# Kernel optimization log

Measured on AMD Instinct MI355X. Metric: run time of the kernel, lower is better.

## Reference

```python
import jax, jax.numpy as jnp
import numpy as np

EMBED_DIM = 1024
NUM_HEADS = 16
HEAD_DIM = EMBED_DIM // NUM_HEADS
LN_EPS = 1e-12
B, S = 2, 2048


def setup_inputs() -> dict:
    key = jax.random.key(0)
    ks = jax.random.split(key, 12)
    scale = 1.0 / np.sqrt(EMBED_DIM)
    d = EMBED_DIM
    return {
        "in_features": jax.random.normal(ks[0], (B, S, d), dtype=jnp.float32),
        "tgt_mask": jnp.ones((B, S), dtype=jnp.float32),
        "Wq": jax.random.normal(ks[1], (d, d), dtype=jnp.float32) * scale,
        "bq": jnp.zeros((d,), dtype=jnp.float32),
        "Wk": jax.random.normal(ks[2], (d, d), dtype=jnp.float32) * scale,
        "bk": jnp.zeros((d,), dtype=jnp.float32),
        "Wv": jax.random.normal(ks[3], (d, d), dtype=jnp.float32) * scale,
        "bv": jnp.zeros((d,), dtype=jnp.float32),
        "Wo": jax.random.normal(ks[4], (d, d), dtype=jnp.float32) * scale,
        "bo": jnp.zeros((d,), dtype=jnp.float32),
        "gamma": jnp.ones((d,), dtype=jnp.float32),
        "beta": jnp.zeros((d,), dtype=jnp.float32),
    }


def _split_heads(x):  # [B,S,D] -> [B,H,S,Dh]
    b, s, _ = x.shape
    return x.reshape(b, s, NUM_HEADS, HEAD_DIM).transpose(0, 2, 1, 3)


def reference(in_features, tgt_mask, Wq, bq, Wk, bk, Wv, bv, Wo, bo, gamma, beta):
    # Self-attention (tgt_features defaults to in_features). Dropout in eval mode (identity).
    q = _split_heads(in_features @ Wq.T + bq)
    k = _split_heads(in_features @ Wk.T + bk)
    v = _split_heads(in_features @ Wv.T + bv)
    # scores: [B,H,S,S]
    scores = jnp.einsum("bhqd,bhkd->bhqk", q, k) / jnp.sqrt(jnp.float32(HEAD_DIM))
    scores = scores + (1.0 - tgt_mask)[:, None, None, :] * (-100000.0)
    attn = jax.nn.softmax(scores, axis=-1)
    ctx = jnp.einsum("bhqk,bhkd->bhqd", attn, v)  # [B,H,S,Dh]
    ctx = ctx.transpose(0, 2, 1, 3).reshape(in_features.shape)  # merge heads
    out = ctx @ Wo.T + bo
    x = out + in_features
    mu = jnp.mean(x, axis=-1, keepdims=True)
    var = jnp.mean(jnp.square(x - mu), axis=-1, keepdims=True)
    return (x - mu) / jnp.sqrt(var + LN_EPS) * gamma + beta
```

## Files before the change

### kernel.cpp

```cpp
#include <hip/hip_runtime.h>
#include <hip/hip_bf16.h>

#define DM   1024
#define HEADS 16
#define DH    64
#define SEQ  2048
#define BATCH   2
#define LOG2E 1.44269504088896f

typedef __attribute__((ext_vector_type(8))) short short8;
typedef __attribute__((ext_vector_type(4))) short bf16x4;
typedef __attribute__((ext_vector_type(4))) float floatx4;

__device__ __forceinline__ short f2b(float f) {
    union { float f; unsigned u; } v; v.f = f;
    unsigned r = v.u + 0x7FFFu + ((v.u >> 16) & 1u);
    return (short)(r >> 16);
}

#if __has_builtin(__builtin_amdgcn_exp2f)
__device__ __forceinline__ float fexp2(float x) { return __builtin_amdgcn_exp2f(x); }
#else
__device__ __forceinline__ float fexp2(float x) { return exp2f(x); }
#endif

__device__ __forceinline__ void async_copy16(const short* gsrc, short* ldst) {
    __builtin_amdgcn_global_load_lds(
        (const __attribute__((address_space(1))) void*)gsrc,
        (__attribute__((address_space(3))) void*)ldst,
        16, 0, 0);
}

__global__ __launch_bounds__(256) void cvt_all(const float* __restrict__ x,
        const float* __restrict__ wq, const float* __restrict__ wk,
        const float* __restrict__ wv, const float* __restrict__ wo,
        const float* __restrict__ mask,
        short* __restrict__ xb, short* __restrict__ wqkv, short* __restrict__ wob,
        float* __restrict__ maddg)
{
    const int b = blockIdx.x;
    if (b >= 8192) {
        const int bb = b - 8192;
        const float* mrow = mask + (size_t)bb * SEQ;
        float* mg = maddg + (size_t)bb * SEQ;
#pragma unroll
        for (int i = 0; i < 8; ++i) {
            const int idx = threadIdx.x * 8 + i;
            mg[idx] = (1.f - mrow[idx]) * (-100000.f * LOG2E);
        }
        return;
    }
    const float* src; short* dst; int idx;
    if (b < 4096)      { src = x;  dst = xb;                idx = b; }
    else if (b < 5120) { src = wq; dst = wqkv;              idx = b - 4096; }
    else if (b < 6144) { src = wk; dst = wqkv + (1 << 20);  idx = b - 5120; }
    else if (b < 7168) { src = wv; dst = wqkv + (2 << 20);  idx = b - 6144; }
    else               { src = wo; dst = wob;               idx = b - 7168; }
    const int i = idx * 256 + threadIdx.x;
    floatx4 v = ((const floatx4*)src)[i];
    bf16x4 o;
    o.x = f2b(v.x); o.y = f2b(v.y); o.z = f2b(v.z); o.w = f2b(v.w);
    ((bf16x4*)dst)[i] = o;
}

__global__ __launch_bounds__(256) void gemm_qkv(const short* __restrict__ A,
        const short* __restrict__ B,
        const float* __restrict__ bq, const float* __restrict__ bk,
        const float* __restrict__ bv,
        short* __restrict__ qw, short* __restrict__ kw, short* __restrict__ vtw)
{
    __shared__ short As[128 * 32];
    __shared__ short Bs[128 * 32];
    const int m0 = blockIdx.x * 128, n0 = blockIdx.y * 128;
    const int w = threadIdx.x >> 6, lane = threadIdx.x & 63;
    const int l16 = lane & 15, quad = lane >> 4;
    const int wm = w >> 1, wn = w & 1;
    const int lr = lane >> 2, lc = (lane & 3) * 8;

    floatx4 acc[4][4];
#pragma unroll
    for (int i = 0; i < 4; ++i)
#pragma unroll
        for (int j = 0; j < 4; ++j) acc[i][j] = (floatx4){0.f, 0.f, 0.f, 0.f};

    for (int kt = 0; kt < DM / 32; ++kt) {
        const int k0 = kt * 32;
        __syncthreads();
        async_copy16(A + (size_t)(m0 + w * 32 + lr) * DM + k0 + lc,      &As[w * 1024]);
        async_copy16(A + (size_t)(m0 + w * 32 + 16 + lr) * DM + k0 + lc, &As[w * 1024 + 512]);
        async_copy16(B + (size_t)(n0 + w * 32 + lr) * DM + k0 + lc,      &Bs[w * 1024]);
        async_copy16(B + (size_t)(n0 + w * 32 + 16 + lr) * DM + k0 + lc, &Bs[w * 1024 + 512]);
        __syncthreads();

        short8 af[4], bf[4];
#pragma unroll
        for (int i = 0; i < 4; ++i)
            af[i] = *(const short8*)&As[(wm * 64 + i * 16 + l16) * 32 + quad * 8];
#pragma unroll
        for (int j = 0; j < 4; ++j)
            bf[j] = *(const short8*)&Bs[(wn * 64 + j * 16 + l16) * 32 + quad * 8];
#pragma unroll
        for (int i = 0; i < 4; ++i)
#pragma unroll
            for (int j = 0; j < 4; ++j)
                acc[i][j] = __builtin_amdgcn_mfma_f32_16x16x32_bf16(af[i], bf[j], acc[i][j], 0, 0, 0);
    }

    const int m_base = m0 + wm * 64 + quad * 4;
#pragma unroll
    for (int j = 0; j < 4; ++j) {
        const int nb = n0 + wn * 64 + j * 16;
        const int t = nb >> 10;
        const int nn = (nb & 1023) + l16;
        const int h = nn >> 6, dh = nn & 63;
        const float* bias = (t == 0) ? bq : (t == 1) ? bk : bv;
        const float bvv = bias[nn];
        if (t == 2) {
#pragma unroll
            for (int i = 0; i < 4; ++i) {
                const int m = m_base + i * 16;
                const int b = m >> 11, s = m & (SEQ - 1);
                bf16x4 p;
                p.x = f2b(acc[i][j][0] + bvv);
                p.y = f2b(acc[i][j][1] + bvv);
                p.z = f2b(acc[i][j][2] + bvv);
                p.w = f2b(acc[i][j][3] + bvv);
                *(bf16x4*)&vtw[(((size_t)(b * HEADS + h)) * DH + dh) * SEQ + s] = p;
            }
        } else {
            short* dst = (t == 0) ? qw : kw;
            const float mulf = (t == 0) ? (0.125f * LOG2E) : 1.0f;
#pragma unroll
            for (int i = 0; i < 4; ++i)
#pragma unroll
                for (int r = 0; r < 4; ++r) {
                    const int m = m_base + i * 16 + r;
                    const int b = m >> 11, s = m & (SEQ - 1);
                    dst[(((size_t)(b * HEADS + h)) * SEQ + s) * DH + dh] =
                        f2b((acc[i][j][r] + bvv) * mulf);
                }
        }
    }
}

__global__ __launch_bounds__(256) void attn_kernel(const short* __restrict__ q,
        const short* __restrict__ k, const short* __restrict__ vt,
        const float* __restrict__ maddg, short* __restrict__ ctx)
{
    const int qtile = blockIdx.x;
    const int bh    = blockIdx.y;
    const int bidx  = bh >> 4;
    const int wave = threadIdx.x >> 6, lane = threadIdx.x & 63;
    const int l16 = lane & 15, quad = lane >> 4;
    const int lx = l16 & 7;

    __shared__ short k_lds[2][64 * 64];
    __shared__ short v_lds[2][64 * 64];
    __shared__ short p_lds[4][16 * 64];

    const int qrow = qtile * 64 + wave * 16 + l16;
    const short* qbase = q + ((size_t)bh * SEQ + qrow) * DH;
    short8 b_q[2];
#pragma unroll
    for (int ks = 0; ks < 2; ++ks)
        b_q[ks] = *(const short8*)(qbase + ks * 32 + quad * 8);

    float m_own = -1e30f;
    floatx4 o[4];
    floatx4 l_acc = (floatx4){0.f, 0.f, 0.f, 0.f};
#pragma unroll
    for (int d = 0; d < 4; ++d) o[d] = (floatx4){0.f, 0.f, 0.f, 0.f};

    short8 ones;
#pragma unroll
    for (int j = 0; j < 8; ++j) ones[j] = (short)0x3F80;

    const short* kbase0 = k  + (size_t)bh * SEQ * DH;
    const short* vbase0 = vt + (size_t)bh * DH * SEQ;
    const float* mrow   = maddg + (size_t)bidx * SEQ;

    const int srow0 = (wave * 64 + lane) >> 3;
    const int srow1 = (256 + wave * 64 + lane) >> 3;
    const int sc    = lane & 7;
    const int g0 = sc ^ (srow0 & 7), g1 = sc ^ (srow1 & 7);

    {
        async_copy16(kbase0 + srow0 * DH + g0 * 8,        &k_lds[0][(wave * 64) * 8]);
        async_copy16(vbase0 + (size_t)srow0 * SEQ + g0 * 8, &v_lds[0][(wave * 64) * 8]);
        async_copy16(kbase0 + srow1 * DH + g1 * 8,        &k_lds[0][(256 + wave * 64) * 8]);
        async_copy16(vbase0 + (size_t)srow1 * SEQ + g1 * 8, &v_lds[0][(256 + wave * 64) * 8]);
    }

    for (int kt = 0; kt < SEQ / 64; ++kt) {
        const int cur = kt & 1;
        __syncthreads();

        floatx4 md[4];
#pragma unroll
        for (int nt = 0; nt < 4; ++nt)
            md[nt] = *(const floatx4*)&mrow[kt * 64 + nt * 16 + quad * 4];

        if (kt + 1 < SEQ / 64) {
            const short* kbase = kbase0 + (size_t)((kt + 1) * 64) * DH;
            const short* vbase = vbase0 + (kt + 1) * 64;
            const int nb = 1 - cur;
            async_copy16(kbase + srow0 * DH + g0 * 8,        &k_lds[nb][(wave * 64) * 8]);
            async_copy16(vbase + (size_t)srow0 * SEQ + g0 * 8, &v_lds[nb][(wave * 64) * 8]);
            async_copy16(kbase + srow1 * DH + g1 * 8,        &k_lds[nb][(256 + wave * 64) * 8]);
            async_copy16(vbase + (size_t)srow1 * SEQ + g1 * 8, &v_lds[nb][(256 + wave * 64) * 8]);
        }

        float sv[4][4];
#pragma unroll
        for (int nt = 0; nt < 4; ++nt) {
            floatx4 acc = md[nt];
#pragma unroll
            for (int ks = 0; ks < 2; ++ks) {
                short8 a = *(const short8*)
                    &k_lds[cur][(nt * 16 + l16) * 64 + (((ks * 4 + quad) ^ lx) * 8)];
                acc = __builtin_amdgcn_mfma_f32_16x16x32_bf16(a, b_q[ks], acc, 0, 0, 0);
            }
#pragma unroll
            for (int r = 0; r < 4; ++r) sv[nt][r] = acc[r];
        }

        float tm = sv[0][0];
#pragma unroll
        for (int nt = 0; nt < 4; ++nt)
#pragma unroll
            for (int r = 0; r < 4; ++r) tm = fmaxf(tm, sv[nt][r]);
        tm = fmaxf(tm, __shfl_xor(tm, 16));
        tm = fmaxf(tm, __shfl_xor(tm, 32));
        const int upd = __any(tm > m_own);
        const float nm = fmaxf(m_own, tm);

#pragma unroll
        for (int nt = 0; nt < 4; ++nt) {
            const float p0 = fexp2(sv[nt][0] - nm);
            const float p1 = fexp2(sv[nt][1] - nm);
            const float p2 = fexp2(sv[nt][2] - nm);
            const float p3 = fexp2(sv[nt][3] - nm);
            union { __hip_bfloat162 h[2]; bf16x4 v; } u;
            u.h[0] = __float22bfloat162_rn(make_float2(p0, p1));
            u.h[1] = __float22bfloat162_rn(make_float2(p2, p3));
            *(bf16x4*)&p_lds[wave][l16 * 64 +
                (((nt * 2 + (quad >> 1)) ^ lx) * 8) + (quad & 1) * 4] = u.v;
        }

        if (upd) {
            const float alpha = fexp2(m_own - nm);
            float ab[4];
#pragma unroll
            for (int r = 0; r < 4; ++r)
                ab[r] = __shfl(alpha, (lane & 48) | (quad * 4 + r));
#pragma unroll
            for (int d = 0; d < 4; ++d)
#pragma unroll
                for (int r = 0; r < 4; ++r) o[d][r] *= ab[r];
#pragma unroll
            for (int r = 0; r < 4; ++r) l_acc[r] *= ab[r];
        }
        m_own = nm;

#pragma unroll
        for (int ks2 = 0; ks2 < 2; ++ks2) {
            short8 pf = *(const short8*)
                &p_lds[wave][l16 * 64 + (((ks2 * 4 + quad) ^ lx) * 8)];
#pragma unroll
            for (int d = 0; d < 4; ++d) {
                short8 vf = *(const short8*)
                    &v_lds[cur][(d * 16 + l16) * 64 + (((ks2 * 4 + quad) ^ lx) * 8)];
                o[d] = __builtin_amdgcn_mfma_f32_16x16x32_bf16(pf, vf, o[d], 0, 0, 0);
            }
            l_acc = __builtin_amdgcn_mfma_f32_16x16x32_bf16(pf, ones, l_acc, 0, 0, 0);
        }
    }

    const int h = bh & 15, bb = bh >> 4;
    const int srow = qtile * 64 + wave * 16 + quad * 4;
    float rl[4];
#pragma unroll
    for (int r = 0; r < 4; ++r) rl[r] = 1.f / l_acc[r];
#pragma unroll
    for (int d = 0; d < 4; ++d) {
        const int dh = d * 16 + l16;
#pragma unroll
        for (int r = 0; r < 4; ++r) {
            const float val = o[d][r] * rl[r];
            ctx[((size_t)(bb * SEQ + srow + r)) * DM + h * 64 + dh] = f2b(val);
        }
    }
}

__global__ __launch_bounds__(256) void gemm_o(const short* __restrict__ A,
        const short* __restrict__ B, const float* __restrict__ bo,
        const float* __restrict__ xin, float* __restrict__ out)
{
    __shared__ short As[128 * 32];
    __shared__ short Bs[128 * 32];
    const int m0 = blockIdx.x * 128, n0 = blockIdx.y * 128;
    const int w = threadIdx.x >> 6, lane = threadIdx.x & 63;
    const int l16 = lane & 15, quad = lane >> 4;
    const int wm = w >> 1, wn = w & 1;
    const int lr = lane >> 2, lc = (lane & 3) * 8;

    floatx4 acc[4][4];
#pragma unroll
    for (int i = 0; i < 4; ++i)
#pragma unroll
        for (int j = 0; j < 4; ++j) acc[i][j] = (floatx4){0.f, 0.f, 0.f, 0.f};

    for (int kt = 0; kt < DM / 32; ++kt) {
        const int k0 = kt * 32;
        __syncthreads();
        async_copy16(A + (size_t)(m0 + w * 32 + lr) * DM + k0 + lc,      &As[w * 1024]);
        async_copy16(A + (size_t)(m0 + w * 32 + 16 + lr) * DM + k0 + lc, &As[w * 1024 + 512]);
        async_copy16(B + (size_t)(n0 + w * 32 + lr) * DM + k0 + lc,      &Bs[w * 1024]);
        async_copy16(B + (size_t)(n0 + w * 32 + 16 + lr) * DM + k0 + lc, &Bs[w * 1024 + 512]);
        __syncthreads();

        short8 af[4], bf[4];
#pragma unroll
        for (int i = 0; i < 4; ++i)
            af[i] = *(const short8*)&As[(wm * 64 + i * 16 + l16) * 32 + quad * 8];
#pragma unroll
        for (int j = 0; j < 4; ++j)
            bf[j] = *(const short8*)&Bs[(wn * 64 + j * 16 + l16) * 32 + quad * 8];
#pragma unroll
        for (int i = 0; i < 4; ++i)
#pragma unroll
            for (int j = 0; j < 4; ++j)
                acc[i][j] = __builtin_amdgcn_mfma_f32_16x16x32_bf16(af[i], bf[j], acc[i][j], 0, 0, 0);
    }

    const int m_base = m0 + wm * 64 + quad * 4;
#pragma unroll
    for (int j = 0; j < 4; ++j) {
        const int n = n0 + wn * 64 + j * 16 + l16;
        const float bvv = bo[n];
#pragma unroll
        for (int i = 0; i < 4; ++i)
#pragma unroll
            for (int r = 0; r < 4; ++r) {
                const int m = m_base + i * 16 + r;
                const size_t idx = (size_t)m * DM + n;
                out[idx] = acc[i][j][r] + bvv + xin[idx];
            }
    }
}

__global__ __launch_bounds__(256) void ln_kernel(float* __restrict__ y,
        const float* __restrict__ gamma, const float* __restrict__ beta)
{
    const int row = blockIdx.x;
    const int t = threadIdx.x;
    const int wave = t >> 6, lane = t & 63;
    const floatx4 v = ((const floatx4*)(y + (size_t)row * DM))[t];
    float s  = v.x + v.y + v.z + v.w;
    float q2 = v.x * v.x + v.y * v.y + v.z * v.z + v.w * v.w;
#pragma unroll
    for (int off = 1; off < 64; off <<= 1) {
        s  += __shfl_xor(s, off);
        q2 += __shfl_xor(q2, off);
    }
    __shared__ float rs[4], rq[4];
    if (lane == 0) { rs[wave] = s; rq[wave] = q2; }
    __syncthreads();
    const float S  = rs[0] + rs[1] + rs[2] + rs[3];
    const float Q2 = rq[0] + rq[1] + rq[2] + rq[3];
    const float mu = S * (1.f / DM);
    float var = Q2 * (1.f / DM) - mu * mu;
    var = fmaxf(var, 0.f);
    const float rstd = rsqrtf(var + 1e-12f);
    const floatx4 g = ((const floatx4*)gamma)[t];
    const floatx4 bt = ((const floatx4*)beta)[t];
    floatx4 o;
    o.x = (v.x - mu) * rstd * g.x + bt.x;
    o.y = (v.y - mu) * rstd * g.y + bt.y;
    o.z = (v.z - mu) * rstd * g.z + bt.z;
    o.w = (v.w - mu) * rstd * g.w + bt.w;
    ((floatx4*)(y + (size_t)row * DM))[t] = o;
}

extern "C" void kernel_launch(void* const* d_in, const int* in_sizes, int n_in,
                              void* d_out, int out_size, void* d_ws, size_t ws_size,
                              hipStream_t stream) {
    const float* x     = (const float*)d_in[0];
    const float* mask  = (const float*)d_in[1];
    const float* Wq    = (const float*)d_in[2];
    const float* bq    = (const float*)d_in[3];
    const float* Wk    = (const float*)d_in[4];
    const float* bk    = (const float*)d_in[5];
    const float* Wv    = (const float*)d_in[6];
    const float* bv    = (const float*)d_in[7];
    const float* Wo    = (const float*)d_in[8];
    const float* bo    = (const float*)d_in[9];
    const float* gamma = (const float*)d_in[10];
    const float* beta  = (const float*)d_in[11];
    float* out = (float*)d_out;

    const size_t NTOK = (size_t)BATCH * SEQ * DM;
    const size_t WSZ  = (size_t)DM * DM;
    short* xb   = (short*)d_ws;
    short* wqkv = xb + NTOK;
    short* wob  = wqkv + 3 * WSZ;
    short* qw   = wob + WSZ;
    short* kw   = qw + NTOK;
    short* vtw  = kw + NTOK;
    short* ctxw = vtw + NTOK;
    float* maddg = (float*)(ctxw + NTOK);

    dim3 blk(256);
    cvt_all<<<dim3(8194), blk, 0, stream>>>(x, Wq, Wk, Wv, Wo, mask, xb, wqkv, wob, maddg);
    gemm_qkv<<<dim3(32, 24), blk, 0, stream>>>(xb, wqkv, bq, bk, bv, qw, kw, vtw);
    attn_kernel<<<dim3(SEQ / 64, BATCH * HEADS), blk, 0, stream>>>(qw, kw, vtw, maddg, ctxw);
    gemm_o<<<dim3(32, 8), blk, 0, stream>>>(ctxw, wob, bo, x, out);
    ln_kernel<<<BATCH * SEQ, blk, 0, stream>>>(out, gamma, beta);
}
```

Baseline: 241.6 us.

## Process two query groups per wave in attention and add separate V transpose

```diff
diff --git a/kernel.cpp b/kernel.cpp
--- a/kernel.cpp
+++ b/kernel.cpp
@@ -67,7 +67,7 @@
         const short* __restrict__ B,
         const float* __restrict__ bq, const float* __restrict__ bk,
         const float* __restrict__ bv,
-        short* __restrict__ qw, short* __restrict__ kw, short* __restrict__ vtw)
+        short* __restrict__ qw, short* __restrict__ kw, short* __restrict__ vw)
 {
     __shared__ short As[128 * 32];
     __shared__ short Bs[128 * 32];
@@ -114,81 +114,97 @@
         const int nn = (nb & 1023) + l16;
         const int h = nn >> 6, dh = nn & 63;
         const float* bias = (t == 0) ? bq : (t == 1) ? bk : bv;
+        short* dst = (t == 0) ? qw : (t == 1) ? kw : vw;
+        const float mulf = (t == 0) ? (0.125f * LOG2E) : 1.0f;
         const float bvv = bias[nn];
-        if (t == 2) {
-#pragma unroll
-            for (int i = 0; i < 4; ++i) {
-                const int m = m_base + i * 16;
+#pragma unroll
+        for (int i = 0; i < 4; ++i)
+#pragma unroll
+            for (int r = 0; r < 4; ++r) {
+                const int m = m_base + i * 16 + r;
                 const int b = m >> 11, s = m & (SEQ - 1);
-                bf16x4 p;
-                p.x = f2b(acc[i][j][0] + bvv);
-                p.y = f2b(acc[i][j][1] + bvv);
-                p.z = f2b(acc[i][j][2] + bvv);
-                p.w = f2b(acc[i][j][3] + bvv);
-                *(bf16x4*)&vtw[(((size_t)(b * HEADS + h)) * DH + dh) * SEQ + s] = p;
-            }
-        } else {
-            short* dst = (t == 0) ? qw : kw;
-            const float mulf = (t == 0) ? (0.125f * LOG2E) : 1.0f;
-#pragma unroll
-            for (int i = 0; i < 4; ++i)
-#pragma unroll
-                for (int r = 0; r < 4; ++r) {
-                    const int m = m_base + i * 16 + r;
-                    const int b = m >> 11, s = m & (SEQ - 1);
-                    dst[(((size_t)(b * HEADS + h)) * SEQ + s) * DH + dh] =
-                        f2b((acc[i][j][r] + bvv) * mulf);
-                }
-        }
-    }
-}
-
-__global__ __launch_bounds__(256) void attn_kernel(const short* __restrict__ q,
+                dst[(((size_t)(b * HEADS + h)) * SEQ + s) * DH + dh] =
+                    f2b((acc[i][j][r] + bvv) * mulf);
+            }
+    }
+}
+
+__global__ __launch_bounds__(256) void transpose_v(const short* __restrict__ v,
+                                                   short* __restrict__ vt)
+{
+    __shared__ short tl[64][72];
+    const int st = blockIdx.x;
+    const int bh = blockIdx.y;
+    const int t = threadIdx.x;
+    const int row = t >> 2, off = (t & 3) * 16;
+    const short* vp = v + ((size_t)bh * SEQ + st * 64 + row) * DH + off;
+    *(short8*)&tl[row][off]     = *(const short8*)vp;
+    *(short8*)&tl[row][off + 8] = *(const short8*)(vp + 8);
+    __syncthreads();
+    short8 o0, o1;
+#pragma unroll
+    for (int j = 0; j < 8; ++j) { o0[j] = tl[off + j][row]; o1[j] = tl[off + 8 + j][row]; }
+    short* op = vt + ((size_t)bh * DH + row) * SEQ + st * 64 + off;
+    *(short8*)op = o0;
+    *(short8*)(op + 8) = o1;
+}
+
+__global__ __launch_bounds__(128) void attn_kernel(const short* __restrict__ q,
         const short* __restrict__ k, const short* __restrict__ vt,
         const float* __restrict__ maddg, short* __restrict__ ctx)
 {
     const int qtile = blockIdx.x;
     const int bh    = blockIdx.y;
     const int bidx  = bh >> 4;
-    const int wave = threadIdx.x >> 6, lane = threadIdx.x & 63;
+    const int tid   = threadIdx.x;
+    const int wave = tid >> 6, lane = tid & 63;
     const int l16 = lane & 15, quad = lane >> 4;
     const int lx = l16 & 7;
 
     __shared__ short k_lds[2][64 * 64];
     __shared__ short v_lds[2][64 * 64];
-    __shared__ short p_lds[4][16 * 64];
-
-    const int qrow = qtile * 64 + wave * 16 + l16;
-    const short* qbase = q + ((size_t)bh * SEQ + qrow) * DH;
-    short8 b_q[2];
-#pragma unroll
-    for (int ks = 0; ks < 2; ++ks)
-        b_q[ks] = *(const short8*)(qbase + ks * 32 + quad * 8);
-
-    float m_own = -1e30f;
-    floatx4 o[4];
-    floatx4 l_acc = (floatx4){0.f, 0.f, 0.f, 0.f};
-#pragma unroll
-    for (int d = 0; d < 4; ++d) o[d] = (floatx4){0.f, 0.f, 0.f, 0.f};
-
-    short8 ones;
-#pragma unroll
-    for (int j = 0; j < 8; ++j) ones[j] = (short)0x3F80;
+    __shared__ short p_lds[2][2][16 * 64];
 
     const short* kbase0 = k  + (size_t)bh * SEQ * DH;
     const short* vbase0 = vt + (size_t)bh * DH * SEQ;
     const float* mrow   = maddg + (size_t)bidx * SEQ;
 
-    const int srow0 = (wave * 64 + lane) >> 3;
-    const int srow1 = (256 + wave * 64 + lane) >> 3;
-    const int sc    = lane & 7;
-    const int g0 = sc ^ (srow0 & 7), g1 = sc ^ (srow1 & 7);
-
-    {
-        async_copy16(kbase0 + srow0 * DH + g0 * 8,        &k_lds[0][(wave * 64) * 8]);
-        async_copy16(vbase0 + (size_t)srow0 * SEQ + g0 * 8, &v_lds[0][(wave * 64) * 8]);
-        async_copy16(kbase0 + srow1 * DH + g1 * 8,        &k_lds[0][(256 + wave * 64) * 8]);
-        async_copy16(vbase0 + (size_t)srow1 * SEQ + g1 * 8, &v_lds[0][(256 + wave * 64) * 8]);
+    short8 b_q[2][2];
+#pragma unroll
+    for (int qg = 0; qg < 2; ++qg) {
+        const int qrow = qtile * 64 + (wave * 2 + qg) * 16 + l16;
+        const short* qb = q + ((size_t)bh * SEQ + qrow) * DH;
+#pragma unroll
+        for (int ks = 0; ks < 2; ++ks)
+            b_q[qg][ks] = *(const short8*)(qb + ks * 32 + quad * 8);
+    }
+
+    float m_own[2] = {-1e30f, -1e30f};
+    floatx4 o[2][4];
+    floatx4 l_acc[2];
+#pragma unroll
+    for (int qg = 0; qg < 2; ++qg) {
+        l_acc[qg] = (floatx4){0.f, 0.f, 0.f, 0.f};
+#pragma unroll
+        for (int d = 0; d < 4; ++d) o[qg][d] = (floatx4){0.f, 0.f, 0.f, 0.f};
+    }
+
+    short8 ones;
+#pragma unroll
+    for (int j = 0; j < 8; ++j) ones[j] = (short)0x3F80;
+
+    int srw[4], gg[4];
+#pragma unroll
+    for (int i = 0; i < 4; ++i) {
+        const int slot = i * 128 + tid;
+        srw[i] = slot >> 3;
+        gg[i]  = (slot & 7) ^ (srw[i] & 7);
+    }
+
+#pragma unroll
+    for (int i = 0; i < 4; ++i) {
+        async_copy16(kbase0 + srw[i] * DH + gg[i] * 8,          &k_lds[0][(i * 128 + tid) * 8]);
+        async_copy16(vbase0 + (size_t)srw[i] * SEQ + gg[i] * 8, &v_lds[0][(i * 128 + tid) * 8]);
     }
 
     for (int kt = 0; kt < SEQ / 64; ++kt) {
@@ -201,93 +217,112 @@
             md[nt] = *(const floatx4*)&mrow[kt * 64 + nt * 16 + quad * 4];
 
         if (kt + 1 < SEQ / 64) {
-            const short* kbase = kbase0 + (size_t)((kt + 1) * 64) * DH;
-            const short* vbase = vbase0 + (kt + 1) * 64;
-            const int nb = 1 - cur;
-            async_copy16(kbase + srow0 * DH + g0 * 8,        &k_lds[nb][(wave * 64) * 8]);
-            async_copy16(vbase + (size_t)srow0 * SEQ + g0 * 8, &v_lds[nb][(wave * 64) * 8]);
-            async_copy16(kbase + srow1 * DH + g1 * 8,        &k_lds[nb][(256 + wave * 64) * 8]);
-            async_copy16(vbase + (size_t)srow1 * SEQ + g1 * 8, &v_lds[nb][(256 + wave * 64) * 8]);
-        }
-
-        float sv[4][4];
+            const short* kb = kbase0 + (size_t)((kt + 1) * 64) * DH;
+            const short* vb = vbase0 + (kt + 1) * 64;
+            const int nb = cur ^ 1;
+#pragma unroll
+            for (int i = 0; i < 4; ++i) {
+                async_copy16(kb + srw[i] * DH + gg[i] * 8,          &k_lds[nb][(i * 128 + tid) * 8]);
+                async_copy16(vb + (size_t)srw[i] * SEQ + gg[i] * 8, &v_lds[nb][(i * 128 + tid) * 8]);
+            }
+        }
+
+        float sv[2][4][4];
 #pragma unroll
         for (int nt = 0; nt < 4; ++nt) {
-            floatx4 acc = md[nt];
+            floatx4 a0 = md[nt], a1 = md[nt];
 #pragma unroll
             for (int ks = 0; ks < 2; ++ks) {
                 short8 a = *(const short8*)
                     &k_lds[cur][(nt * 16 + l16) * 64 + (((ks * 4 + quad) ^ lx) * 8)];
-                acc = __builtin_amdgcn_mfma_f32_16x16x32_bf16(a, b_q[ks], acc, 0, 0, 0);
-            }
-#pragma unroll
-            for (int r = 0; r < 4; ++r) sv[nt][r] = acc[r];
-        }
-
-        float tm = sv[0][0];
-#pragma unroll
-        for (int nt = 0; nt < 4; ++nt)
-#pragma unroll
-            for (int r = 0; r < 4; ++r) tm = fmaxf(tm, sv[nt][r]);
-        tm = fmaxf(tm, __shfl_xor(tm, 16));
-        tm = fmaxf(tm, __shfl_xor(tm, 32));
-        const int upd = __any(tm > m_own);
-        const float nm = fmaxf(m_own, tm);
-
-#pragma unroll
-        for (int nt = 0; nt < 4; ++nt) {
-            const float p0 = fexp2(sv[nt][0] - nm);
-            const float p1 = fexp2(sv[nt][1] - nm);
-            const float p2 = fexp2(sv[nt][2] - nm);
-            const float p3 = fexp2(sv[nt][3] - nm);
-            union { __hip_bfloat162 h[2]; bf16x4 v; } u;
-            u.h[0] = __float22bfloat162_rn(make_float2(p0, p1));
-            u.h[1] = __float22bfloat162_rn(make_float2(p2, p3));
-            *(bf16x4*)&p_lds[wave][l16 * 64 +
-                (((nt * 2 + (quad >> 1)) ^ lx) * 8) + (quad & 1) * 4] = u.v;
-        }
+                a0 = __builtin_amdgcn_mfma_f32_16x16x32_bf16(a, b_q[0][ks], a0, 0, 0, 0);
+                a1 = __builtin_amdgcn_mfma_f32_16x16x32_bf16(a, b_q[1][ks], a1, 0, 0, 0);
+            }
+#pragma unroll
+            for (int r = 0; r < 4; ++r) { sv[0][nt][r] = a0[r]; sv[1][nt][r] = a1[r]; }
+        }
+
+        float tmv[2], nm[2];
+#pragma unroll
+        for (int qg = 0; qg < 2; ++qg) {
+            float tm = sv[qg][0][0];
+#pragma unroll
+            for (int nt = 0; nt < 4; ++nt)
+#pragma unroll
+                for (int r = 0; r < 4; ++r) tm = fmaxf(tm, sv[qg][nt][r]);
+            tm = fmaxf(tm, __shfl_xor(tm, 16));
+            tm = fmaxf(tm, __shfl_xor(tm, 32));
+            tmv[qg] = tm;
+            nm[qg] = fmaxf(m_own[qg], tm);
+        }
+        const int upd = __any((tmv[0] > m_own[0]) | (tmv[1] > m_own[1]));
+
+#pragma unroll
+        for (int qg = 0; qg < 2; ++qg)
+#pragma unroll
+            for (int nt = 0; nt < 4; ++nt) {
+                const float p0 = fexp2(sv[qg][nt][0] - nm[qg]);
+                const float p1 = fexp2(sv[qg][nt][1] - nm[qg]);
+                const float p2 = fexp2(sv[qg][nt][2] - nm[qg]);
+                const float p3 = fexp2(sv[qg][nt][3] - nm[qg]);
+                union { __hip_bfloat162 h[2]; bf16x4 v; } u;
+                u.h[0] = __float22bfloat162_rn(make_float2(p0, p1));
+                u.h[1] = __float22bfloat162_rn(make_float2(p2, p3));
+                *(bf16x4*)&p_lds[wave][qg][l16 * 64 +
+                    (((nt * 2 + (quad >> 1)) ^ lx) * 8) + (quad & 1) * 4] = u.v;
+            }
 
         if (upd) {
-            const float alpha = fexp2(m_own - nm);
-            float ab[4];
-#pragma unroll
-            for (int r = 0; r < 4; ++r)
-                ab[r] = __shfl(alpha, (lane & 48) | (quad * 4 + r));
-#pragma unroll
-            for (int d = 0; d < 4; ++d)
-#pragma unroll
-                for (int r = 0; r < 4; ++r) o[d][r] *= ab[r];
-#pragma unroll
-            for (int r = 0; r < 4; ++r) l_acc[r] *= ab[r];
-        }
-        m_own = nm;
+#pragma unroll
+            for (int qg = 0; qg < 2; ++qg) {
+                const float alpha = fexp2(m_own[qg] - nm[qg]);
+                float ab[4];
+#pragma unroll
+                for (int r = 0; r < 4; ++r)
+                    ab[r] = __shfl(alpha, (lane & 48) | (quad * 4 + r));
+#pragma unroll
+                for (int d = 0; d < 4; ++d)
+#pragma unroll
+                    for (int r = 0; r < 4; ++r) o[qg][d][r] *= ab[r];
+#pragma unroll
+                for (int r = 0; r < 4; ++r) l_acc[qg][r] *= ab[r];
+            }
+        }
+        m_own[0] = nm[0]; m_own[1] = nm[1];
 
 #pragma unroll
         for (int ks2 = 0; ks2 < 2; ++ks2) {
-            short8 pf = *(const short8*)
-                &p_lds[wave][l16 * 64 + (((ks2 * 4 + quad) ^ lx) * 8)];
+            short8 pf0 = *(const short8*)
+                &p_lds[wave][0][l16 * 64 + (((ks2 * 4 + quad) ^ lx) * 8)];
+            short8 pf1 = *(const short8*)
+                &p_lds[wave][1][l16 * 64 + (((ks2 * 4 + quad) ^ lx) * 8)];
 #pragma unroll
             for (int d = 0; d < 4; ++d) {
                 short8 vf = *(const short8*)
                     &v_lds[cur][(d * 16 + l16) * 64 + (((ks2 * 4 + quad) ^ lx) * 8)];
-                o[d] = __builtin_amdgcn_mfma_f32_16x16x32_bf16(pf, vf, o[d], 0, 0, 0);
-            }
-            l_acc = __builtin_amdgcn_mfma_f32_16x16x32_bf16(pf, ones, l_acc, 0, 0, 0);
+                o[0][d] = __builtin_amdgcn_mfma_f32_16x16x32_bf16(pf0, vf, o[0][d], 0, 0, 0);
+                o[1][d] = __builtin_amdgcn_mfma_f32_16x16x32_bf16(pf1, vf, o[1][d], 0, 0, 0);
+            }
+            l_acc[0] = __builtin_amdgcn_mfma_f32_16x16x32_bf16(pf0, ones, l_acc[0], 0, 0, 0);
+            l_acc[1] = __builtin_amdgcn_mfma_f32_16x16x32_bf16(pf1, ones, l_acc[1], 0, 0, 0);
         }
     }
 
     const int h = bh & 15, bb = bh >> 4;
-    const int srow = qtile * 64 + wave * 16 + quad * 4;
-    float rl[4];
-#pragma unroll
-    for (int r = 0; r < 4; ++r) rl[r] = 1.f / l_acc[r];
-#pragma unroll
-    for (int d = 0; d < 4; ++d) {
-        const int dh = d * 16 + l16;
-#pragma unroll
-        for (int r = 0; r < 4; ++r) {
-            const float val = o[d][r] * rl[r];
-            ctx[((size_t)(bb * SEQ + srow + r)) * DM + h * 64 + dh] = f2b(val);
+#pragma unroll
+    for (int qg = 0; qg < 2; ++qg) {
+        const int srow = qtile * 64 + (wave * 2 + qg) * 16 + quad * 4;
+        float rl[4];
+#pragma unroll
+        for (int r = 0; r < 4; ++r) rl[r] = 1.f / l_acc[qg][r];
+#pragma unroll
+        for (int d = 0; d < 4; ++d) {
+            const int dh = d * 16 + l16;
+#pragma unroll
+            for (int r = 0; r < 4; ++r) {
+                const float val = o[qg][d][r] * rl[r];
+                ctx[((size_t)(bb * SEQ + srow + r)) * DM + h * 64 + dh] = f2b(val);
+            }
         }
     }
 }
@@ -406,14 +441,16 @@
     short* wob  = wqkv + 3 * WSZ;
     short* qw   = wob + WSZ;
     short* kw   = qw + NTOK;
-    short* vtw  = kw + NTOK;
-    short* ctxw = vtw + NTOK;
-    float* maddg = (float*)(ctxw + NTOK);
+    short* vw   = kw + NTOK;
+    short* vtw  = vw + NTOK;
+    short* ctxw = vw;
+    float* maddg = (float*)(vtw + NTOK);
 
     dim3 blk(256);
     cvt_all<<<dim3(8194), blk, 0, stream>>>(x, Wq, Wk, Wv, Wo, mask, xb, wqkv, wob, maddg);
-    gemm_qkv<<<dim3(32, 24), blk, 0, stream>>>(xb, wqkv, bq, bk, bv, qw, kw, vtw);
-    attn_kernel<<<dim3(SEQ / 64, BATCH * HEADS), blk, 0, stream>>>(qw, kw, vtw, maddg, ctxw);
+    gemm_qkv<<<dim3(32, 24), blk, 0, stream>>>(xb, wqkv, bq, bk, bv, qw, kw, vw);
+    transpose_v<<<dim3(SEQ / 64, BATCH * HEADS), blk, 0, stream>>>(vw, vtw);
+    attn_kernel<<<dim3(SEQ / 64, BATCH * HEADS), dim3(128), 0, stream>>>(qw, kw, vtw, maddg, ctxw);
     gemm_o<<<dim3(32, 8), blk, 0, stream>>>(ctxw, wob, bo, x, out);
     ln_kernel<<<BATCH * SEQ, blk, 0, stream>>>(out, gamma, beta);
 }
```

After: 240.9 us. Within noise of the previous version (-0.3%).
